# Kernel optimization log

Hardware: AMD Instinct MI355X
Metric: run time of the kernel (lower is better)

## Reference

```python
import math
import jax, jax.numpy as jnp
import numpy as np

LMAX = 2


def _cg_complex(j1, m1, j2, m2, j3, m3):
    # Standard (Racah) Clebsch-Gordan coefficient <j1 m1 j2 m2 | j3 m3> for integer l.
    if m1 + m2 != m3 or j3 < abs(j1 - j2) or j3 > j1 + j2:
        return 0.0
    f = math.factorial
    pre = math.sqrt((2 * j3 + 1) * f(j3 + j1 - j2) * f(j3 - j1 + j2) * f(j1 + j2 - j3) / f(j1 + j2 + j3 + 1))
    pre *= math.sqrt(f(j3 + m3) * f(j3 - m3) * f(j1 - m1) * f(j1 + m1) * f(j2 - m2) * f(j2 + m2))
    kmin = max(0, j2 - j3 - m1, j1 + m2 - j3)
    kmax = min(j1 + j2 - j3, j1 - m1, j2 + m2)
    s = 0.0
    for k in range(kmin, kmax + 1):
        s += (-1.0) ** k / (f(k) * f(j1 + j2 - j3 - k) * f(j1 - m1 - k) * f(j2 + m2 - k) * f(j3 - j2 + m1 + k) * f(j3 - j1 - m2 + k))
    return pre * s


def _u_matrix(l):
    # Unitary map from complex SH (Condon-Shortley) to real SH, rows = real mu, cols = complex m.
    U = np.zeros((2 * l + 1, 2 * l + 1), dtype=np.complex128)
    U[l, l] = 1.0
    isq2 = 1.0 / math.sqrt(2.0)
    for m in range(1, l + 1):
        U[l + m, l - m] = isq2
        U[l + m, l + m] = ((-1.0) ** m) * isq2
        U[l - m, l - m] = 1j * isq2
        U[l - m, l + m] = -1j * ((-1.0) ** m) * isq2
    return U


def _real_clebsch_gordan(lmax):
    # Dense real-SH CG tensor over combined s=(l,m) indices, shape [S,S,S], S=(lmax+1)^2.
    S = (lmax + 1) ** 2
    cg = np.zeros((S, S, S))
    for l1 in range(lmax + 1):
        for l2 in range(lmax + 1):
            for l3 in range(abs(l1 - l2), min(lmax, l1 + l2) + 1):
                blk = np.zeros((2 * l1 + 1, 2 * l2 + 1, 2 * l3 + 1))
                for i1, m1 in enumerate(range(-l1, l1 + 1)):
                    for i2, m2 in enumerate(range(-l2, l2 + 1)):
                        for i3, m3 in enumerate(range(-l3, l3 + 1)):
                            blk[i1, i2, i3] = _cg_complex(l1, m1, l2, m2, l3, m3)
                U1, U2, U3 = _u_matrix(l1), _u_matrix(l2), _u_matrix(l3)
                r = np.einsum('am,bn,co,mno->abc', U1, U2, U3.conj(), blk.astype(np.complex128))
                r = r.real if (l1 + l2 + l3) % 2 == 0 else r.imag  # parity-dependent real part
                cg[l1 * l1:(l1 + 1) ** 2, l2 * l2:(l2 + 1) ** 2, l3 * l3:(l3 + 1) ** 2] = r
    return cg


def _sparse_cg(lmax):
    cg = _real_clebsch_gordan(lmax)
    i1, i2, i3 = np.nonzero(np.abs(cg) > 1e-10)
    vals = cg[i1, i2, i3].astype(np.float32)
    widx = np.floor(np.sqrt(i3.astype(np.float64))).astype(np.int32)  # l of output combined index
    return vals, i1.astype(np.int32), i2.astype(np.int32), i3.astype(np.int32), widx


def _spherical_harmonics_l2(d):
    # Real SH up to l=2, 'component' normalization (|x|=1 assumed). Order: (l,m) = (0,0),(1,-1),(1,0),(1,1),(2,-2..2).
    x, y, z = d[..., 0], d[..., 1], d[..., 2]
    s3, s5, s15 = math.sqrt(3.0), math.sqrt(5.0), math.sqrt(15.0)
    return jnp.stack([
        jnp.ones_like(x),
        s3 * y, s3 * z, s3 * x,
        s15 * x * y, s15 * y * z, 0.5 * s5 * (3.0 * z * z - 1.0), s15 * x * z, 0.5 * s15 * (x * x - y * y),
    ], axis=-1)


def setup_inputs():
    N_ATOMS, N_EDGES, N_BASIS, N_RADIAL = 1200, 12000, 128, 20
    S = (LMAX + 1) ** 2
    key = jax.random.key(0)
    ks = jax.random.split(key, 8)
    vals, i1, i2, i3, widx = _sparse_cg(LMAX)
    return {
        'x': jax.random.normal(ks[0], (N_ATOMS, S, N_BASIS), jnp.float32),
        'radial_ij': jax.random.uniform(ks[1], (N_EDGES, N_RADIAL), jnp.float32),
        'dir_ij': jax.random.normal(ks[2], (N_EDGES, 3), jnp.float32),
        'cutoff_ij': jax.random.uniform(ks[3], (N_EDGES, 1), jnp.float32),
        'W_filter': jax.random.normal(ks[6], (N_RADIAL, N_BASIS * (LMAX + 1)), jnp.float32) / math.sqrt(N_RADIAL),
        'b_filter': jnp.zeros((N_BASIS * (LMAX + 1),), jnp.float32),
        'cg_vals': jnp.asarray(vals),
        'idx_i': jax.random.randint(ks[4], (N_EDGES,), 0, N_ATOMS),
        'idx_j': jax.random.randint(ks[5], (N_EDGES,), 0, N_ATOMS),
        'cg_idx_in1': jnp.asarray(i1),
        'cg_idx_in2': jnp.asarray(i2),
        'cg_idx_out': jnp.asarray(i3),
        'w_idx': jnp.asarray(widx),
    }


def reference(x, radial_ij, dir_ij, cutoff_ij, W_filter, b_filter, cg_vals,
              idx_i, idx_j, cg_idx_in1, cg_idx_in2, cg_idx_out, w_idx):
    n_atoms, S, F = x.shape
    E = dir_ij.shape[0]
    d = dir_ij / jnp.linalg.norm(dir_ij, axis=-1, keepdims=True)
    Y = _spherical_harmonics_l2(d)                        # [E, S]
    Wij = (radial_ij @ W_filter + b_filter) * cutoff_ij   # [E, (lmax+1)*F]
    Wij = Wij.reshape(E, LMAX + 1, F)                     # per-l radial filter
    xj = x[idx_j]                                         # [E, S, F] neighbor features
    # Sparse CG tensor-product contraction over combined (l,m) indices.
    v = (Y[:, cg_idx_in2, None] * cg_vals[None, :, None]
         * Wij[:, w_idx, :] * xj[:, cg_idx_in1, :])       # [E, n_cg, F]
    yij = jnp.zeros((E, S, F), v.dtype).at[:, cg_idx_out, :].add(v)
    return jax.ops.segment_sum(yij, idx_i, num_segments=n_atoms)
```

## Files before the change

### kernel.cpp

```cpp
#include <hip/hip_runtime.h>
#include <math.h>


#define S9     9
#define MROW   12
#define NF     128
#define NRAD   20
#define TEDGE  8
#define MAXA   2048
#define EMAX   12288

__device__ inline float2 f2fma(float a, float2 b, float2 c) {
    return make_float2(fmaf(a, b.x, c.x), fmaf(a, b.y, c.y));
}

__global__ __launch_bounds__(1024) void csr_kernel(
    const int* __restrict__ idx_i, int E, int A,
    int* __restrict__ offsets,
    int* __restrict__ esorted)
{
    __shared__ int lcnt[MAXA];
    __shared__ int wtot[16];
    __shared__ int esh[EMAX];
    const int t = threadIdx.x;
    const int lane = t & 63;
    const int wid  = t >> 6;

    for (int i = t; i < A; i += 1024) lcnt[i] = 0;
    __syncthreads();
    for (int e = t; e < E; e += 1024) atomicAdd(&lcnt[idx_i[e]], 1);
    __syncthreads();

    const int i0 = 2 * t, i1 = 2 * t + 1;
    const int ca = (i0 < A) ? lcnt[i0] : 0;
    const int cb = (i1 < A) ? lcnt[i1] : 0;
    __syncthreads();

    int inc = ca + cb;
    #pragma unroll
    for (int d = 1; d < 64; d <<= 1) {
        int u = __shfl_up(inc, d);
        if (lane >= d) inc += u;
    }
    if (lane == 63) wtot[wid] = inc;
    __syncthreads();
    if (wid == 0) {
        int w = (lane < 16) ? wtot[lane] : 0;
        #pragma unroll
        for (int d = 1; d < 16; d <<= 1) {
            int u = __shfl_up(w, d);
            if (lane >= d) w += u;
        }
        if (lane < 16) wtot[lane] = w;
    }
    __syncthreads();
    int run = ((wid > 0) ? wtot[wid - 1] : 0) + (inc - (ca + cb));
    if (i0 < A) { offsets[i0] = run; lcnt[i0] = run; run += ca; }
    if (i1 < A) { offsets[i1] = run; lcnt[i1] = run; run += cb; }
    if (t == 1023) offsets[A] = wtot[15];
    __syncthreads();

    if (E <= EMAX) {
        for (int e = t; e < E; e += 1024) {
            int p = atomicAdd(&lcnt[idx_i[e]], 1);
            esh[p] = e;
        }
        __syncthreads();
        for (int i = t; i < E; i += 1024) esorted[i] = esh[i];
    } else {
        for (int e = t; e < E; e += 1024) {
            int p = atomicAdd(&lcnt[idx_i[e]], 1);
            esorted[p] = e;
        }
    }
}

__global__ __launch_bounds__(64) void so3_atom_kernel(
    const float* __restrict__ x,
    const float* __restrict__ radial,
    const float* __restrict__ dir,
    const float* __restrict__ cutoff,
    const float* __restrict__ Wf,
    const float* __restrict__ bf,
    const float* __restrict__ cg_vals,
    const int* __restrict__ idx_j,
    const int* __restrict__ cg_i1,
    const int* __restrict__ cg_i2,
    const int* __restrict__ cg_i3,
    int ncg,
    const int* __restrict__ offsets,
    const int* __restrict__ esorted,
    float* __restrict__ out)
{
    const int a = blockIdx.x;
    const int t = threadIdx.x;
    const int e0 = offsets[a];
    const int e1 = offsets[a + 1];

    __shared__ __align__(16) float M[TEDGE][MROW * S9];
    __shared__ float Ysh[TEDGE][S9];
    __shared__ float radsh[TEDGE][NRAD];
    __shared__ float cutsh[TEDGE];
    __shared__ int   jsh[TEDGE];

    float2 acc[S9];
    #pragma unroll
    for (int s = 0; s < S9; ++s) acc[s] = make_float2(0.f, 0.f);

    const float2 b0 = ((const float2*)(bf + 0 * NF))[t];
    const float2 b1 = ((const float2*)(bf + 1 * NF))[t];
    const float2 b2 = ((const float2*)(bf + 2 * NF))[t];

    for (int base = e0; base < e1; base += TEDGE) {
        const int n = min(TEDGE, e1 - base);

        {
            float4* Mz = (float4*)&M[0][0];
            const int tot4 = TEDGE * MROW * S9 / 4;
            for (int qq = t; qq < tot4; qq += 64) Mz[qq] = make_float4(0.f, 0.f, 0.f, 0.f);
        }
        if (t < TEDGE) {
            int jj = a;
            float cut = 0.f;
            if (t < n) {
                const int e = esorted[base + t];
                jj = idx_j[e];
                cut = cutoff[e];
                float dx = dir[3 * e], dy = dir[3 * e + 1], dz = dir[3 * e + 2];
                const float inv = rsqrtf(dx * dx + dy * dy + dz * dz);
                dx *= inv; dy *= inv; dz *= inv;
                const float s3c  = 1.7320508075688772f;
                const float s5c  = 2.2360679774997896f;
                const float s15c = 3.8729833462074170f;
                Ysh[t][0] = 1.0f;
                Ysh[t][1] = s3c * dy;
                Ysh[t][2] = s3c * dz;
                Ysh[t][3] = s3c * dx;
                Ysh[t][4] = s15c * dx * dy;
                Ysh[t][5] = s15c * dy * dz;
                Ysh[t][6] = 0.5f * s5c * (3.0f * dz * dz - 1.0f);
                Ysh[t][7] = s15c * dx * dz;
                Ysh[t][8] = 0.5f * s15c * (dx * dx - dy * dy);
            }
            jsh[t] = jj;
            cutsh[t] = cut;
        }
        for (int qq = t; qq < TEDGE * NRAD; qq += 64) {
            const int c = qq / NRAD;
            const int r = qq - c * NRAD;
            radsh[c][r] = (c < n) ? radial[(size_t)esorted[base + c] * NRAD + r] : 0.f;
        }
        __syncthreads();

        float2 w[TEDGE][3];
        #pragma unroll
        for (int c = 0; c < TEDGE; ++c) { w[c][0] = b0; w[c][1] = b1; w[c][2] = b2; }
        #pragma unroll 4
        for (int r = 0; r < NRAD; ++r) {
            const float2* wrow = (const float2*)(Wf + r * (3 * NF));
            const float2 w0 = wrow[t];
            const float2 w1 = wrow[t + 64];
            const float2 w2 = wrow[t + 128];
            #pragma unroll
            for (int c = 0; c < TEDGE; ++c) {
                const float rv = radsh[c][r];
                w[c][0] = f2fma(rv, w0, w[c][0]);
                w[c][1] = f2fma(rv, w1, w[c][1]);
                w[c][2] = f2fma(rv, w2, w[c][2]);
            }
        }
        #pragma unroll
        for (int c = 0; c < TEDGE; ++c) {
            const float cut = cutsh[c];
            w[c][0].x *= cut; w[c][0].y *= cut;
            w[c][1].x *= cut; w[c][1].y *= cut;
            w[c][2].x *= cut; w[c][2].y *= cut;
        }

        {
            const int c = t >> 3;
            const int r = t & 7;
            if (c < n) {
                for (int kk = r; kk < ncg; kk += 8) {
                    atomicAdd(&M[c][cg_i3[kk] * MROW + cg_i1[kk]], cg_vals[kk] * Ysh[c][cg_i2[kk]]);
                }
            }
        }
        __syncthreads();

        #pragma unroll
        for (int c = 0; c < TEDGE; ++c) {
            const int j = __builtin_amdgcn_readfirstlane(jsh[c]);

            const float2* xp = (const float2*)(x + (size_t)j * (S9 * NF)) + t;
            float2 xj[S9];
            #pragma unroll
            for (int s = 0; s < S9; ++s) xj[s] = xp[s * 64];

            #pragma unroll
            for (int s3 = 0; s3 < S9; ++s3) {
                const float4* mr = (const float4*)&M[c][s3 * MROW];
                const float4 m0 = mr[0];
                const float4 m1 = mr[1];
                const float  m8 = M[c][s3 * MROW + 8];
                float2 tsum = make_float2(0.f, 0.f);
                tsum = f2fma(m0.x, xj[0], tsum);
                tsum = f2fma(m0.y, xj[1], tsum);
                tsum = f2fma(m0.z, xj[2], tsum);
                tsum = f2fma(m0.w, xj[3], tsum);
                tsum = f2fma(m1.x, xj[4], tsum);
                tsum = f2fma(m1.y, xj[5], tsum);
                tsum = f2fma(m1.z, xj[6], tsum);
                tsum = f2fma(m1.w, xj[7], tsum);
                tsum = f2fma(m8,   xj[8], tsum);
                const float2 wl = (s3 == 0) ? w[c][0] : ((s3 < 4) ? w[c][1] : w[c][2]);
                acc[s3].x = fmaf(wl.x, tsum.x, acc[s3].x);
                acc[s3].y = fmaf(wl.y, tsum.y, acc[s3].y);
            }
        }
        __syncthreads();
    }

    float2* op = (float2*)(out + (size_t)a * (S9 * NF)) + t;
    #pragma unroll
    for (int s = 0; s < S9; ++s) op[s * 64] = acc[s];
}

extern "C" void kernel_launch(void* const* d_in, const int* in_sizes, int n_in,
                              void* d_out, int out_size, void* d_ws, size_t ws_size,
                              hipStream_t stream) {
    const float* x       = (const float*)d_in[0];
    const float* radial  = (const float*)d_in[1];
    const float* dir     = (const float*)d_in[2];
    const float* cutoff  = (const float*)d_in[3];
    const float* Wf      = (const float*)d_in[4];
    const float* bf      = (const float*)d_in[5];
    const float* cg_vals = (const float*)d_in[6];
    const int*   idx_i   = (const int*)d_in[7];
    const int*   idx_j   = (const int*)d_in[8];
    const int*   cg_i1   = (const int*)d_in[9];
    const int*   cg_i2   = (const int*)d_in[10];
    const int*   cg_i3   = (const int*)d_in[11];

    const int E   = in_sizes[7];
    const int ncg = in_sizes[6];
    const int A   = in_sizes[0] / (S9 * NF);

    int* offsets = (int*)d_ws;
    int* esorted = offsets + (A + 1);

    csr_kernel<<<1, 1024, 0, stream>>>(idx_i, E, A, offsets, esorted);

    so3_atom_kernel<<<A, 64, 0, stream>>>(
        x, radial, dir, cutoff, Wf, bf, cg_vals, idx_j,
        cg_i1, cg_i2, cg_i3, ncg, offsets, esorted, (float*)d_out);
}
```

Measured before the change: 137.3 us.

## Split each atom's edge tiles across four waves and reduce through shared memory

The per-atom kernel grows from one 64-lane wave to four waves per block. Each wave processes interleaved tiles of eight edges with its own shared-memory staging buffers. At the end the partial accumulators are reduced through the reused M buffer before one write. The aim is more parallelism and latency hiding per atom, which matters when there are few atoms or many edges per atom. The cost is more shared memory per block, block-wide syncs that idle waves with no tile left, and an extra reduction step.

```diff
diff --git a/kernel.cpp b/kernel.cpp
--- a/kernel.cpp
+++ b/kernel.cpp
@@ -7,6 +7,7 @@
 #define NF     128
 #define NRAD   20
 #define TEDGE  8
+#define WAVES  4
 #define MAXA   2048
 #define EMAX   12288
 
@@ -75,7 +76,7 @@
     }
 }
 
-__global__ __launch_bounds__(64) void so3_atom_kernel(
+__global__ __launch_bounds__(256) void so3_atom_kernel(
     const float* __restrict__ x,
     const float* __restrict__ radial,
     const float* __restrict__ dir,
@@ -94,36 +95,42 @@
 {
     const int a = blockIdx.x;
     const int t = threadIdx.x;
+    const int lane = t & 63;
+    const int wid  = t >> 6;
     const int e0 = offsets[a];
     const int e1 = offsets[a + 1];
-
-    __shared__ __align__(16) float M[TEDGE][MROW * S9];
-    __shared__ float Ysh[TEDGE][S9];
-    __shared__ float radsh[TEDGE][NRAD];
-    __shared__ float cutsh[TEDGE];
-    __shared__ int   jsh[TEDGE];
+    const int T = (e1 - e0 + TEDGE - 1) / TEDGE;
+    const int K = (T + WAVES - 1) / WAVES;
+
+    __shared__ __align__(16) float M[WAVES][TEDGE][MROW * S9];
+    __shared__ float Ysh[WAVES][TEDGE][S9];
+    __shared__ float radsh[WAVES][TEDGE][NRAD];
+    __shared__ float cutsh[WAVES][TEDGE];
+    __shared__ int   jsh[WAVES][TEDGE];
 
     float2 acc[S9];
     #pragma unroll
     for (int s = 0; s < S9; ++s) acc[s] = make_float2(0.f, 0.f);
 
-    const float2 b0 = ((const float2*)(bf + 0 * NF))[t];
-    const float2 b1 = ((const float2*)(bf + 1 * NF))[t];
-    const float2 b2 = ((const float2*)(bf + 2 * NF))[t];
-
-    for (int base = e0; base < e1; base += TEDGE) {
-        const int n = min(TEDGE, e1 - base);
+    const float2 b0 = ((const float2*)(bf + 0 * NF))[lane];
+    const float2 b1 = ((const float2*)(bf + 1 * NF))[lane];
+    const float2 b2 = ((const float2*)(bf + 2 * NF))[lane];
+
+    for (int k = 0; k < K; ++k) {
+        const int tile = k * WAVES + wid;
+        const int base = e0 + tile * TEDGE;
+        const int n = min(TEDGE, max(0, e1 - base));
 
         {
-            float4* Mz = (float4*)&M[0][0];
+            float4* Mz = (float4*)&M[wid][0][0];
             const int tot4 = TEDGE * MROW * S9 / 4;
-            for (int qq = t; qq < tot4; qq += 64) Mz[qq] = make_float4(0.f, 0.f, 0.f, 0.f);
-        }
-        if (t < TEDGE) {
+            for (int qq = lane; qq < tot4; qq += 64) Mz[qq] = make_float4(0.f, 0.f, 0.f, 0.f);
+        }
+        if (lane < TEDGE) {
             int jj = a;
             float cut = 0.f;
-            if (t < n) {
-                const int e = esorted[base + t];
+            if (lane < n) {
+                const int e = esorted[base + lane];
                 jj = idx_j[e];
                 cut = cutoff[e];
                 float dx = dir[3 * e], dy = dir[3 * e + 1], dz = dir[3 * e + 2];
@@ -132,23 +139,23 @@
                 const float s3c  = 1.7320508075688772f;
                 const float s5c  = 2.2360679774997896f;
                 const float s15c = 3.8729833462074170f;
-                Ysh[t][0] = 1.0f;
-                Ysh[t][1] = s3c * dy;
-                Ysh[t][2] = s3c * dz;
-                Ysh[t][3] = s3c * dx;
-                Ysh[t][4] = s15c * dx * dy;
-                Ysh[t][5] = s15c * dy * dz;
-                Ysh[t][6] = 0.5f * s5c * (3.0f * dz * dz - 1.0f);
-                Ysh[t][7] = s15c * dx * dz;
-                Ysh[t][8] = 0.5f * s15c * (dx * dx - dy * dy);
-            }
-            jsh[t] = jj;
-            cutsh[t] = cut;
-        }
-        for (int qq = t; qq < TEDGE * NRAD; qq += 64) {
+                Ysh[wid][lane][0] = 1.0f;
+                Ysh[wid][lane][1] = s3c * dy;
+                Ysh[wid][lane][2] = s3c * dz;
+                Ysh[wid][lane][3] = s3c * dx;
+                Ysh[wid][lane][4] = s15c * dx * dy;
+                Ysh[wid][lane][5] = s15c * dy * dz;
+                Ysh[wid][lane][6] = 0.5f * s5c * (3.0f * dz * dz - 1.0f);
+                Ysh[wid][lane][7] = s15c * dx * dz;
+                Ysh[wid][lane][8] = 0.5f * s15c * (dx * dx - dy * dy);
+            }
+            jsh[wid][lane] = jj;
+            cutsh[wid][lane] = cut;
+        }
+        for (int qq = lane; qq < TEDGE * NRAD; qq += 64) {
             const int c = qq / NRAD;
             const int r = qq - c * NRAD;
-            radsh[c][r] = (c < n) ? radial[(size_t)esorted[base + c] * NRAD + r] : 0.f;
+            radsh[wid][c][r] = (c < n) ? radial[(size_t)esorted[base + c] * NRAD + r] : 0.f;
         }
         __syncthreads();
 
@@ -158,12 +165,12 @@
         #pragma unroll 4
         for (int r = 0; r < NRAD; ++r) {
             const float2* wrow = (const float2*)(Wf + r * (3 * NF));
-            const float2 w0 = wrow[t];
-            const float2 w1 = wrow[t + 64];
-            const float2 w2 = wrow[t + 128];
+            const float2 w0 = wrow[lane];
+            const float2 w1 = wrow[lane + 64];
+            const float2 w2 = wrow[lane + 128];
             #pragma unroll
             for (int c = 0; c < TEDGE; ++c) {
-                const float rv = radsh[c][r];
+                const float rv = radsh[wid][c][r];
                 w[c][0] = f2fma(rv, w0, w[c][0]);
                 w[c][1] = f2fma(rv, w1, w[c][1]);
                 w[c][2] = f2fma(rv, w2, w[c][2]);
@@ -171,18 +178,19 @@
         }
         #pragma unroll
         for (int c = 0; c < TEDGE; ++c) {
-            const float cut = cutsh[c];
+            const float cut = cutsh[wid][c];
             w[c][0].x *= cut; w[c][0].y *= cut;
             w[c][1].x *= cut; w[c][1].y *= cut;
             w[c][2].x *= cut; w[c][2].y *= cut;
         }
 
         {
-            const int c = t >> 3;
-            const int r = t & 7;
+            const int c = lane >> 3;
+            const int r = lane & 7;
             if (c < n) {
                 for (int kk = r; kk < ncg; kk += 8) {
-                    atomicAdd(&M[c][cg_i3[kk] * MROW + cg_i1[kk]], cg_vals[kk] * Ysh[c][cg_i2[kk]]);
+                    atomicAdd(&M[wid][c][cg_i3[kk] * MROW + cg_i1[kk]],
+                              cg_vals[kk] * Ysh[wid][c][cg_i2[kk]]);
                 }
             }
         }
@@ -190,19 +198,19 @@
 
         #pragma unroll
         for (int c = 0; c < TEDGE; ++c) {
-            const int j = __builtin_amdgcn_readfirstlane(jsh[c]);
-
-            const float2* xp = (const float2*)(x + (size_t)j * (S9 * NF)) + t;
+            const int j = __builtin_amdgcn_readfirstlane(jsh[wid][c]);
+
+            const float2* xp = (const float2*)(x + (size_t)j * (S9 * NF)) + lane;
             float2 xj[S9];
             #pragma unroll
             for (int s = 0; s < S9; ++s) xj[s] = xp[s * 64];
 
             #pragma unroll
             for (int s3 = 0; s3 < S9; ++s3) {
-                const float4* mr = (const float4*)&M[c][s3 * MROW];
+                const float4* mr = (const float4*)&M[wid][c][s3 * MROW];
                 const float4 m0 = mr[0];
                 const float4 m1 = mr[1];
-                const float  m8 = M[c][s3 * MROW + 8];
+                const float  m8 = M[wid][c][s3 * MROW + 8];
                 float2 tsum = make_float2(0.f, 0.f);
                 tsum = f2fma(m0.x, xj[0], tsum);
                 tsum = f2fma(m0.y, xj[1], tsum);
@@ -221,9 +229,27 @@
         __syncthreads();
     }
 
-    float2* op = (float2*)(out + (size_t)a * (S9 * NF)) + t;
-    #pragma unroll
-    for (int s = 0; s < S9; ++s) op[s * 64] = acc[s];
+    float* red = &M[0][0][0];
+    if (wid > 0) {
+        float2* rp = (float2*)(red + (size_t)(wid - 1) * (S9 * NF)) + lane;
+        #pragma unroll
+        for (int s = 0; s < S9; ++s) rp[s * 64] = acc[s];
+    }
+    __syncthreads();
+    if (wid == 0) {
+        #pragma unroll
+        for (int r2 = 0; r2 < WAVES - 1; ++r2) {
+            const float2* rp = (const float2*)(red + (size_t)r2 * (S9 * NF)) + lane;
+            #pragma unroll
+            for (int s = 0; s < S9; ++s) {
+                float2 v = rp[s * 64];
+                acc[s].x += v.x; acc[s].y += v.y;
+            }
+        }
+        float2* op = (float2*)(out + (size_t)a * (S9 * NF)) + lane;
+        #pragma unroll
+        for (int s = 0; s < S9; ++s) op[s * 64] = acc[s];
+    }
 }
 
 extern "C" void kernel_launch(void* const* d_in, const int* in_sizes, int n_in,
@@ -251,7 +277,7 @@
 
     csr_kernel<<<1, 1024, 0, stream>>>(idx_i, E, A, offsets, esorted);
 
-    so3_atom_kernel<<<A, 64, 0, stream>>>(
+    so3_atom_kernel<<<A, 256, 0, stream>>>(
         x, radial, dir, cutoff, Wf, bf, cg_vals, idx_j,
         cg_i1, cg_i2, cg_i3, ncg, offsets, esorted, (float*)d_out);
 }
```

Result: slower. 169.6 us (+23.5%).

## Split feature dimension across two blocks per atom and batch neighbor gathers

Applied to the files above, without the earlier changes.

Each atom is now processed by two 64-thread blocks, each owning half of the 128 features with one float per thread instead of a float2. This doubles the grid size to improve occupancy and latency hiding on a GPU with many compute units. The neighbor feature loads are also grouped four edges at a time to issue more independent memory requests. The cost is that the per-edge setup work (spherical harmonics, CG matrix build with shared atomics, radial loads) is now done twice per atom, and global loads are narrower.

```diff
diff --git a/kernel.cpp b/kernel.cpp
--- a/kernel.cpp
+++ b/kernel.cpp
@@ -9,10 +9,6 @@
 #define TEDGE  8
 #define MAXA   2048
 #define EMAX   12288
-
-__device__ inline float2 f2fma(float a, float2 b, float2 c) {
-    return make_float2(fmaf(a, b.x, c.x), fmaf(a, b.y, c.y));
-}
 
 __global__ __launch_bounds__(1024) void csr_kernel(
     const int* __restrict__ idx_i, int E, int A,
@@ -92,8 +88,10 @@
     const int* __restrict__ esorted,
     float* __restrict__ out)
 {
-    const int a = blockIdx.x;
-    const int t = threadIdx.x;
+    const int a  = blockIdx.x >> 1;
+    const int fh = blockIdx.x & 1;
+    const int t  = threadIdx.x;
+    const int f  = fh * 64 + t;
     const int e0 = offsets[a];
     const int e1 = offsets[a + 1];
 
@@ -103,13 +101,13 @@
     __shared__ float cutsh[TEDGE];
     __shared__ int   jsh[TEDGE];
 
-    float2 acc[S9];
+    float acc[S9];
     #pragma unroll
-    for (int s = 0; s < S9; ++s) acc[s] = make_float2(0.f, 0.f);
-
-    const float2 b0 = ((const float2*)(bf + 0 * NF))[t];
-    const float2 b1 = ((const float2*)(bf + 1 * NF))[t];
-    const float2 b2 = ((const float2*)(bf + 2 * NF))[t];
+    for (int s = 0; s < S9; ++s) acc[s] = 0.f;
+
+    const float b0 = bf[0 * NF + f];
+    const float b1 = bf[1 * NF + f];
+    const float b2 = bf[2 * NF + f];
 
     for (int base = e0; base < e1; base += TEDGE) {
         const int n = min(TEDGE, e1 - base);
@@ -152,29 +150,27 @@
         }
         __syncthreads();
 
-        float2 w[TEDGE][3];
+        float w[TEDGE][3];
         #pragma unroll
         for (int c = 0; c < TEDGE; ++c) { w[c][0] = b0; w[c][1] = b1; w[c][2] = b2; }
         #pragma unroll 4
         for (int r = 0; r < NRAD; ++r) {
-            const float2* wrow = (const float2*)(Wf + r * (3 * NF));
-            const float2 w0 = wrow[t];
-            const float2 w1 = wrow[t + 64];
-            const float2 w2 = wrow[t + 128];
+            const float* wrow = Wf + r * (3 * NF) + f;
+            const float w0 = wrow[0];
+            const float w1 = wrow[NF];
+            const float w2 = wrow[2 * NF];
             #pragma unroll
             for (int c = 0; c < TEDGE; ++c) {
                 const float rv = radsh[c][r];
-                w[c][0] = f2fma(rv, w0, w[c][0]);
-                w[c][1] = f2fma(rv, w1, w[c][1]);
-                w[c][2] = f2fma(rv, w2, w[c][2]);
+                w[c][0] = fmaf(rv, w0, w[c][0]);
+                w[c][1] = fmaf(rv, w1, w[c][1]);
+                w[c][2] = fmaf(rv, w2, w[c][2]);
             }
         }
         #pragma unroll
         for (int c = 0; c < TEDGE; ++c) {
             const float cut = cutsh[c];
-            w[c][0].x *= cut; w[c][0].y *= cut;
-            w[c][1].x *= cut; w[c][1].y *= cut;
-            w[c][2].x *= cut; w[c][2].y *= cut;
+            w[c][0] *= cut; w[c][1] *= cut; w[c][2] *= cut;
         }
 
         {
@@ -182,48 +178,52 @@
             const int r = t & 7;
             if (c < n) {
                 for (int kk = r; kk < ncg; kk += 8) {
-                    atomicAdd(&M[c][cg_i3[kk] * MROW + cg_i1[kk]], cg_vals[kk] * Ysh[c][cg_i2[kk]]);
+                    atomicAdd(&M[c][cg_i3[kk] * MROW + cg_i1[kk]],
+                              cg_vals[kk] * Ysh[c][cg_i2[kk]]);
                 }
             }
         }
         __syncthreads();
 
         #pragma unroll
-        for (int c = 0; c < TEDGE; ++c) {
-            const int j = __builtin_amdgcn_readfirstlane(jsh[c]);
-
-            const float2* xp = (const float2*)(x + (size_t)j * (S9 * NF)) + t;
-            float2 xj[S9];
+        for (int g = 0; g < 2; ++g) {
+            float xj[4][S9];
             #pragma unroll
-            for (int s = 0; s < S9; ++s) xj[s] = xp[s * 64];
-
+            for (int c2 = 0; c2 < 4; ++c2) {
+                const int j = __builtin_amdgcn_readfirstlane(jsh[g * 4 + c2]);
+                const float* xp = x + (size_t)j * (S9 * NF) + f;
+                #pragma unroll
+                for (int s = 0; s < S9; ++s) xj[c2][s] = xp[s * NF];
+            }
             #pragma unroll
-            for (int s3 = 0; s3 < S9; ++s3) {
-                const float4* mr = (const float4*)&M[c][s3 * MROW];
-                const float4 m0 = mr[0];
-                const float4 m1 = mr[1];
-                const float  m8 = M[c][s3 * MROW + 8];
-                float2 tsum = make_float2(0.f, 0.f);
-                tsum = f2fma(m0.x, xj[0], tsum);
-                tsum = f2fma(m0.y, xj[1], tsum);
-                tsum = f2fma(m0.z, xj[2], tsum);
-                tsum = f2fma(m0.w, xj[3], tsum);
-                tsum = f2fma(m1.x, xj[4], tsum);
-                tsum = f2fma(m1.y, xj[5], tsum);
-                tsum = f2fma(m1.z, xj[6], tsum);
-                tsum = f2fma(m1.w, xj[7], tsum);
-                tsum = f2fma(m8,   xj[8], tsum);
-                const float2 wl = (s3 == 0) ? w[c][0] : ((s3 < 4) ? w[c][1] : w[c][2]);
-                acc[s3].x = fmaf(wl.x, tsum.x, acc[s3].x);
-                acc[s3].y = fmaf(wl.y, tsum.y, acc[s3].y);
-            }
-        }
-        __syncthreads();
-    }
-
-    float2* op = (float2*)(out + (size_t)a * (S9 * NF)) + t;
+            for (int c2 = 0; c2 < 4; ++c2) {
+                const int c = g * 4 + c2;
+                #pragma unroll
+                for (int s3 = 0; s3 < S9; ++s3) {
+                    const float4* mr = (const float4*)&M[c][s3 * MROW];
+                    const float4 m0 = mr[0];
+                    const float4 m1 = mr[1];
+                    const float  m8 = M[c][s3 * MROW + 8];
+                    float ts = m0.x * xj[c2][0];
+                    ts = fmaf(m0.y, xj[c2][1], ts);
+                    ts = fmaf(m0.z, xj[c2][2], ts);
+                    ts = fmaf(m0.w, xj[c2][3], ts);
+                    ts = fmaf(m1.x, xj[c2][4], ts);
+                    ts = fmaf(m1.y, xj[c2][5], ts);
+                    ts = fmaf(m1.z, xj[c2][6], ts);
+                    ts = fmaf(m1.w, xj[c2][7], ts);
+                    ts = fmaf(m8,   xj[c2][8], ts);
+                    const float wl = (s3 == 0) ? w[c][0] : ((s3 < 4) ? w[c][1] : w[c][2]);
+                    acc[s3] = fmaf(wl, ts, acc[s3]);
+                }
+            }
+        }
+        __syncthreads();
+    }
+
+    float* op = out + (size_t)a * (S9 * NF) + f;
     #pragma unroll
-    for (int s = 0; s < S9; ++s) op[s * 64] = acc[s];
+    for (int s = 0; s < S9; ++s) op[s * NF] = acc[s];
 }
 
 extern "C" void kernel_launch(void* const* d_in, const int* in_sizes, int n_in,
@@ -251,7 +251,7 @@
 
     csr_kernel<<<1, 1024, 0, stream>>>(idx_i, E, A, offsets, esorted);
 
-    so3_atom_kernel<<<A, 64, 0, stream>>>(
+    so3_atom_kernel<<<2 * A, 64, 0, stream>>>(
         x, radial, dir, cutoff, Wf, bf, cg_vals, idx_j,
         cg_i1, cg_i2, cg_i3, ncg, offsets, esorted, (float*)d_out);
 }
```

Result: slower. 146.6 us (+6.8%).

## Replace CSR sort and per-atom gather with edge-parallel kernel using global atomics

Applied to the files above, without the earlier changes.

Drops the single-block CSR sort kernel and the per-atom gather kernel. One fused kernel now assigns one wavefront per edge, with four edges per block. Each wave builds its CG matrix in its own shared-memory slice, computes the radial filter from per-lane radial values, and scatters its result into the output with float atomicAdd. The output is zeroed first with a memset. This removes the serial single-block sort and the per-atom load imbalance, at the cost of many global float atomics, contention on popular target atoms, and a summation order that is no longer deterministic.

```diff
diff --git a/kernel.cpp b/kernel.cpp
--- a/kernel.cpp
+++ b/kernel.cpp
@@ -4,78 +4,16 @@
 
 #define S9     9
 #define MROW   12
+#define MSZ    (S9 * MROW)
 #define NF     128
 #define NRAD   20
-#define TEDGE  8
-#define MAXA   2048
-#define EMAX   12288
+#define EPB    4
 
 __device__ inline float2 f2fma(float a, float2 b, float2 c) {
     return make_float2(fmaf(a, b.x, c.x), fmaf(a, b.y, c.y));
 }
 
-__global__ __launch_bounds__(1024) void csr_kernel(
-    const int* __restrict__ idx_i, int E, int A,
-    int* __restrict__ offsets,
-    int* __restrict__ esorted)
-{
-    __shared__ int lcnt[MAXA];
-    __shared__ int wtot[16];
-    __shared__ int esh[EMAX];
-    const int t = threadIdx.x;
-    const int lane = t & 63;
-    const int wid  = t >> 6;
-
-    for (int i = t; i < A; i += 1024) lcnt[i] = 0;
-    __syncthreads();
-    for (int e = t; e < E; e += 1024) atomicAdd(&lcnt[idx_i[e]], 1);
-    __syncthreads();
-
-    const int i0 = 2 * t, i1 = 2 * t + 1;
-    const int ca = (i0 < A) ? lcnt[i0] : 0;
-    const int cb = (i1 < A) ? lcnt[i1] : 0;
-    __syncthreads();
-
-    int inc = ca + cb;
-    #pragma unroll
-    for (int d = 1; d < 64; d <<= 1) {
-        int u = __shfl_up(inc, d);
-        if (lane >= d) inc += u;
-    }
-    if (lane == 63) wtot[wid] = inc;
-    __syncthreads();
-    if (wid == 0) {
-        int w = (lane < 16) ? wtot[lane] : 0;
-        #pragma unroll
-        for (int d = 1; d < 16; d <<= 1) {
-            int u = __shfl_up(w, d);
-            if (lane >= d) w += u;
-        }
-        if (lane < 16) wtot[lane] = w;
-    }
-    __syncthreads();
-    int run = ((wid > 0) ? wtot[wid - 1] : 0) + (inc - (ca + cb));
-    if (i0 < A) { offsets[i0] = run; lcnt[i0] = run; run += ca; }
-    if (i1 < A) { offsets[i1] = run; lcnt[i1] = run; run += cb; }
-    if (t == 1023) offsets[A] = wtot[15];
-    __syncthreads();
-
-    if (E <= EMAX) {
-        for (int e = t; e < E; e += 1024) {
-            int p = atomicAdd(&lcnt[idx_i[e]], 1);
-            esh[p] = e;
-        }
-        __syncthreads();
-        for (int i = t; i < E; i += 1024) esorted[i] = esh[i];
-    } else {
-        for (int e = t; e < E; e += 1024) {
-            int p = atomicAdd(&lcnt[idx_i[e]], 1);
-            esorted[p] = e;
-        }
-    }
-}
-
-__global__ __launch_bounds__(64) void so3_atom_kernel(
+__global__ __launch_bounds__(256) void so3_edge_fused(
     const float* __restrict__ x,
     const float* __restrict__ radial,
     const float* __restrict__ dir,
@@ -83,147 +21,95 @@
     const float* __restrict__ Wf,
     const float* __restrict__ bf,
     const float* __restrict__ cg_vals,
+    const int* __restrict__ idx_i,
     const int* __restrict__ idx_j,
     const int* __restrict__ cg_i1,
     const int* __restrict__ cg_i2,
     const int* __restrict__ cg_i3,
-    int ncg,
-    const int* __restrict__ offsets,
-    const int* __restrict__ esorted,
+    int ncg, int E,
     float* __restrict__ out)
 {
-    const int a = blockIdx.x;
-    const int t = threadIdx.x;
-    const int e0 = offsets[a];
-    const int e1 = offsets[a + 1];
+    const int wid  = threadIdx.x >> 6;
+    const int lane = threadIdx.x & 63;
+    const int e = blockIdx.x * EPB + wid;
+    if (e >= E) return;
 
-    __shared__ __align__(16) float M[TEDGE][MROW * S9];
-    __shared__ float Ysh[TEDGE][S9];
-    __shared__ float radsh[TEDGE][NRAD];
-    __shared__ float cutsh[TEDGE];
-    __shared__ int   jsh[TEDGE];
+    __shared__ __align__(16) float Msh[EPB][MSZ];
+    __shared__ float Ysh[EPB][S9];
 
-    float2 acc[S9];
-    #pragma unroll
-    for (int s = 0; s < S9; ++s) acc[s] = make_float2(0.f, 0.f);
+    if (lane < 27) ((float4*)&Msh[wid][0])[lane] = make_float4(0.f, 0.f, 0.f, 0.f);
 
-    const float2 b0 = ((const float2*)(bf + 0 * NF))[t];
-    const float2 b1 = ((const float2*)(bf + 1 * NF))[t];
-    const float2 b2 = ((const float2*)(bf + 2 * NF))[t];
-
-    for (int base = e0; base < e1; base += TEDGE) {
-        const int n = min(TEDGE, e1 - base);
-
-        {
-            float4* Mz = (float4*)&M[0][0];
-            const int tot4 = TEDGE * MROW * S9 / 4;
-            for (int qq = t; qq < tot4; qq += 64) Mz[qq] = make_float4(0.f, 0.f, 0.f, 0.f);
-        }
-        if (t < TEDGE) {
-            int jj = a;
-            float cut = 0.f;
-            if (t < n) {
-                const int e = esorted[base + t];
-                jj = idx_j[e];
-                cut = cutoff[e];
-                float dx = dir[3 * e], dy = dir[3 * e + 1], dz = dir[3 * e + 2];
-                const float inv = rsqrtf(dx * dx + dy * dy + dz * dz);
-                dx *= inv; dy *= inv; dz *= inv;
-                const float s3c  = 1.7320508075688772f;
-                const float s5c  = 2.2360679774997896f;
-                const float s15c = 3.8729833462074170f;
-                Ysh[t][0] = 1.0f;
-                Ysh[t][1] = s3c * dy;
-                Ysh[t][2] = s3c * dz;
-                Ysh[t][3] = s3c * dx;
-                Ysh[t][4] = s15c * dx * dy;
-                Ysh[t][5] = s15c * dy * dz;
-                Ysh[t][6] = 0.5f * s5c * (3.0f * dz * dz - 1.0f);
-                Ysh[t][7] = s15c * dx * dz;
-                Ysh[t][8] = 0.5f * s15c * (dx * dx - dy * dy);
-            }
-            jsh[t] = jj;
-            cutsh[t] = cut;
-        }
-        for (int qq = t; qq < TEDGE * NRAD; qq += 64) {
-            const int c = qq / NRAD;
-            const int r = qq - c * NRAD;
-            radsh[c][r] = (c < n) ? radial[(size_t)esorted[base + c] * NRAD + r] : 0.f;
-        }
-        __syncthreads();
-
-        float2 w[TEDGE][3];
-        #pragma unroll
-        for (int c = 0; c < TEDGE; ++c) { w[c][0] = b0; w[c][1] = b1; w[c][2] = b2; }
-        #pragma unroll 4
-        for (int r = 0; r < NRAD; ++r) {
-            const float2* wrow = (const float2*)(Wf + r * (3 * NF));
-            const float2 w0 = wrow[t];
-            const float2 w1 = wrow[t + 64];
-            const float2 w2 = wrow[t + 128];
-            #pragma unroll
-            for (int c = 0; c < TEDGE; ++c) {
-                const float rv = radsh[c][r];
-                w[c][0] = f2fma(rv, w0, w[c][0]);
-                w[c][1] = f2fma(rv, w1, w[c][1]);
-                w[c][2] = f2fma(rv, w2, w[c][2]);
-            }
-        }
-        #pragma unroll
-        for (int c = 0; c < TEDGE; ++c) {
-            const float cut = cutsh[c];
-            w[c][0].x *= cut; w[c][0].y *= cut;
-            w[c][1].x *= cut; w[c][1].y *= cut;
-            w[c][2].x *= cut; w[c][2].y *= cut;
-        }
-
-        {
-            const int c = t >> 3;
-            const int r = t & 7;
-            if (c < n) {
-                for (int kk = r; kk < ncg; kk += 8) {
-                    atomicAdd(&M[c][cg_i3[kk] * MROW + cg_i1[kk]], cg_vals[kk] * Ysh[c][cg_i2[kk]]);
-                }
-            }
-        }
-        __syncthreads();
-
-        #pragma unroll
-        for (int c = 0; c < TEDGE; ++c) {
-            const int j = __builtin_amdgcn_readfirstlane(jsh[c]);
-
-            const float2* xp = (const float2*)(x + (size_t)j * (S9 * NF)) + t;
-            float2 xj[S9];
-            #pragma unroll
-            for (int s = 0; s < S9; ++s) xj[s] = xp[s * 64];
-
-            #pragma unroll
-            for (int s3 = 0; s3 < S9; ++s3) {
-                const float4* mr = (const float4*)&M[c][s3 * MROW];
-                const float4 m0 = mr[0];
-                const float4 m1 = mr[1];
-                const float  m8 = M[c][s3 * MROW + 8];
-                float2 tsum = make_float2(0.f, 0.f);
-                tsum = f2fma(m0.x, xj[0], tsum);
-                tsum = f2fma(m0.y, xj[1], tsum);
-                tsum = f2fma(m0.z, xj[2], tsum);
-                tsum = f2fma(m0.w, xj[3], tsum);
-                tsum = f2fma(m1.x, xj[4], tsum);
-                tsum = f2fma(m1.y, xj[5], tsum);
-                tsum = f2fma(m1.z, xj[6], tsum);
-                tsum = f2fma(m1.w, xj[7], tsum);
-                tsum = f2fma(m8,   xj[8], tsum);
-                const float2 wl = (s3 == 0) ? w[c][0] : ((s3 < 4) ? w[c][1] : w[c][2]);
-                acc[s3].x = fmaf(wl.x, tsum.x, acc[s3].x);
-                acc[s3].y = fmaf(wl.y, tsum.y, acc[s3].y);
-            }
-        }
-        __syncthreads();
+    float dx = dir[3 * e], dy = dir[3 * e + 1], dz = dir[3 * e + 2];
+    const float inv = rsqrtf(dx * dx + dy * dy + dz * dz);
+    dx *= inv; dy *= inv; dz *= inv;
+    if (lane == 0) {
+        const float s3c  = 1.7320508075688772f;
+        const float s5c  = 2.2360679774997896f;
+        const float s15c = 3.8729833462074170f;
+        Ysh[wid][0] = 1.0f;
+        Ysh[wid][1] = s3c * dy;
+        Ysh[wid][2] = s3c * dz;
+        Ysh[wid][3] = s3c * dx;
+        Ysh[wid][4] = s15c * dx * dy;
+        Ysh[wid][5] = s15c * dy * dz;
+        Ysh[wid][6] = 0.5f * s5c * (3.0f * dz * dz - 1.0f);
+        Ysh[wid][7] = s15c * dx * dz;
+        Ysh[wid][8] = 0.5f * s15c * (dx * dx - dy * dy);
     }
 
-    float2* op = (float2*)(out + (size_t)a * (S9 * NF)) + t;
+    for (int k = lane; k < ncg; k += 64) {
+        atomicAdd(&Msh[wid][cg_i3[k] * MROW + cg_i1[k]],
+                  cg_vals[k] * Ysh[wid][cg_i2[k]]);
+    }
+
+    float rad[NRAD];
     #pragma unroll
-    for (int s = 0; s < S9; ++s) op[s * 64] = acc[s];
+    for (int r = 0; r < NRAD; ++r) rad[r] = radial[(size_t)e * NRAD + r];
+    const float cut = cutoff[e];
+
+    float2 w0 = ((const float2*)(bf + 0 * NF))[lane];
+    float2 w1 = ((const float2*)(bf + 1 * NF))[lane];
+    float2 w2 = ((const float2*)(bf + 2 * NF))[lane];
+    #pragma unroll 4
+    for (int r = 0; r < NRAD; ++r) {
+        const float2* wrow = (const float2*)(Wf + r * (3 * NF));
+        w0 = f2fma(rad[r], wrow[lane],       w0);
+        w1 = f2fma(rad[r], wrow[lane + 64],  w1);
+        w2 = f2fma(rad[r], wrow[lane + 128], w2);
+    }
+    w0.x *= cut; w0.y *= cut;
+    w1.x *= cut; w1.y *= cut;
+    w2.x *= cut; w2.y *= cut;
+
+    const int j = __builtin_amdgcn_readfirstlane(idx_j[e]);
+    const float2* xp = (const float2*)(x + (size_t)j * (S9 * NF)) + lane;
+    float2 xj[S9];
+    #pragma unroll
+    for (int s = 0; s < S9; ++s) xj[s] = xp[s * 64];
+
+    const int a = __builtin_amdgcn_readfirstlane(idx_i[e]);
+    float* op = out + (size_t)a * (S9 * NF) + 2 * lane;
+
+    #pragma unroll
+    for (int s3 = 0; s3 < S9; ++s3) {
+        const float4* mr = (const float4*)&Msh[wid][s3 * MROW];
+        const float4 m0 = mr[0];
+        const float4 m1 = mr[1];
+        const float  m8 = Msh[wid][s3 * MROW + 8];
+        float2 tsum = make_float2(0.f, 0.f);
+        tsum = f2fma(m0.x, xj[0], tsum);
+        tsum = f2fma(m0.y, xj[1], tsum);
+        tsum = f2fma(m0.z, xj[2], tsum);
+        tsum = f2fma(m0.w, xj[3], tsum);
+        tsum = f2fma(m1.x, xj[4], tsum);
+        tsum = f2fma(m1.y, xj[5], tsum);
+        tsum = f2fma(m1.z, xj[6], tsum);
+        tsum = f2fma(m1.w, xj[7], tsum);
+        tsum = f2fma(m8,   xj[8], tsum);
+        const float2 wl = (s3 == 0) ? w0 : ((s3 < 4) ? w1 : w2);
+        atomicAdd(&op[s3 * NF],     wl.x * tsum.x);
+        atomicAdd(&op[s3 * NF + 1], wl.y * tsum.y);
+    }
 }
 
 extern "C" void kernel_launch(void* const* d_in, const int* in_sizes, int n_in,
@@ -244,14 +130,10 @@
 
     const int E   = in_sizes[7];
     const int ncg = in_sizes[6];
-    const int A   = in_sizes[0] / (S9 * NF);
 
-    int* offsets = (int*)d_ws;
-    int* esorted = offsets + (A + 1);
+    hipMemsetAsync(d_out, 0, (size_t)out_size * sizeof(float), stream);
 
-    csr_kernel<<<1, 1024, 0, stream>>>(idx_i, E, A, offsets, esorted);
-
-    so3_atom_kernel<<<A, 64, 0, stream>>>(
-        x, radial, dir, cutoff, Wf, bf, cg_vals, idx_j,
-        cg_i1, cg_i2, cg_i3, ncg, offsets, esorted, (float*)d_out);
+    so3_edge_fused<<<(E + EPB - 1) / EPB, 64 * EPB, 0, stream>>>(
+        x, radial, dir, cutoff, Wf, bf, cg_vals, idx_i, idx_j,
+        cg_i1, cg_i2, cg_i3, ncg, E, (float*)d_out);
 }
```

After: 181.7 us. 1.32x slower.
